# Performance work log

Measured on AMD Instinct MI355X. Metric: run time of the kernel, lower is better.

## Reference

```python
import jax, jax.numpy as jnp
import numpy as np

N_NODES = 100000
N_FEAT = 512
HIDDEN = 256
N_CLASSES = 40
N_EDGES = 1600000
K = 10
ALPHA = 0.1


def setup_inputs() -> dict:
    key = jax.random.key(0)
    ks = jax.random.split(key, 8)
    feat = jax.random.normal(ks[0], (N_NODES, N_FEAT), dtype=jnp.float32)
    src = jax.random.randint(ks[1], (N_EDGES,), 0, N_NODES, dtype=jnp.int32)
    dst = jax.random.randint(ks[2], (N_EDGES,), 0, N_NODES, dtype=jnp.int32)
    # linear layers (PyTorch-style uniform init)
    s1 = 1.0 / np.sqrt(N_FEAT)
    W1 = jax.random.uniform(ks[3], (N_FEAT, HIDDEN), minval=-s1, maxval=s1, dtype=jnp.float32)
    b1 = jax.random.uniform(ks[4], (HIDDEN,), minval=-s1, maxval=s1, dtype=jnp.float32)
    s2 = 1.0 / np.sqrt(HIDDEN)
    W2 = jax.random.uniform(ks[5], (HIDDEN, N_CLASSES), minval=-s2, maxval=s2, dtype=jnp.float32)
    b2 = jax.random.uniform(ks[6], (N_CLASSES,), minval=-s2, maxval=s2, dtype=jnp.float32)
    # PPR init for per-hop weights: temp[k] = alpha*(1-alpha)^k, temp[K] = (1-alpha)^K
    temp = ALPHA * (1.0 - ALPHA) ** np.arange(K + 1)
    temp[-1] = (1.0 - ALPHA) ** K
    temp = jnp.asarray(temp, dtype=jnp.float32)
    return {"feat": feat, "W1": W1, "b1": b1, "W2": W2, "b2": b2,
            "temp": temp, "src": src, "dst": dst}


def reference(feat, W1, b1, W2, b2, temp, src, dst):
    N = feat.shape[0]
    # dgl.add_self_loop
    loop = jnp.arange(N, dtype=src.dtype)
    src_f = jnp.concatenate([src, loop])
    dst_f = jnp.concatenate([dst, loop])
    # MLP: lin1 -> relu -> lin2 (dropout is identity at inference)
    h = jax.nn.relu(feat @ W1 + b1) @ W2 + b2  # [N, C]
    # symmetric normalization: norm_e = d[dst] * d[src], d = deg^{-1/2}
    deg = jax.ops.segment_sum(jnp.ones_like(dst_f, dtype=h.dtype), dst_f, num_segments=N)
    d = jax.lax.rsqrt(deg)  # deg >= 1 due to self loops
    norm = (d[dst_f] * d[src_f])[:, None]  # [E, 1]
    # K-hop propagation with learned per-hop weights
    TH = h * temp[0]
    for k in range(K):
        msg = h[src_f] * norm                     # gather + edge scale
        h = jax.ops.segment_sum(msg, dst_f, num_segments=N)  # scatter-sum
        TH = TH + h * temp[k + 1]
    return jax.nn.log_softmax(TH, axis=1)
```

## Files before the change

kernel.cpp:

```cpp
#include <hip/hip_runtime.h>
#include <math.h>

#define N_NODES 100000
#define N_FEAT  512
#define HIDDEN  256
#define N_CLS   40
#define N_EDGES 1600000
#define K_HOPS  10

#define NPART   8
#define PSZ     12500
#define NPN     (NPART * N_NODES)
#define SCANB   782
#define HROW    40

typedef __attribute__((ext_vector_type(8))) short short8;
typedef __attribute__((ext_vector_type(4))) float f4_t;

__device__ __forceinline__ short f2bf(float f) {
    union { float f; unsigned u; } x; x.f = f;
    unsigned r = x.u + 0x7fffu + ((x.u >> 16) & 1u);
    return (short)(r >> 16);
}

__device__ __forceinline__ float bf2f(short b) {
    union { unsigned u; float f; } x;
    x.u = ((unsigned)(unsigned short)b) << 16;
    return x.f;
}


__global__ __launch_bounds__(256) void init_degp_kernel(int* __restrict__ degp) {
    int idx = blockIdx.x * 256 + threadIdx.x;
    if (idx < NPN) {
        int v = idx >> 3, p = idx & 7;
        degp[idx] = (p == v / PSZ) ? 1 : 0;
    }
}

__global__ __launch_bounds__(256) void count_dst_kernel(const int* __restrict__ src,
                                                        const int* __restrict__ dst,
                                                        int* __restrict__ degp) {
    int e = blockIdx.x * 256 + threadIdx.x;
    if (e < N_EDGES) atomicAdd(&degp[dst[e] * NPART + src[e] / PSZ], 1);
}

__global__ __launch_bounds__(256) void rsqrt_deg_kernel(const int* __restrict__ degp,
                                                        float* __restrict__ d) {
    int v = blockIdx.x * 256 + threadIdx.x;
    if (v < N_NODES) {
        int s = 0;
#pragma unroll
        for (int p = 0; p < NPART; ++p) s += degp[v * NPART + p];
        d[v] = rsqrtf((float)s);
    }
}


__global__ __launch_bounds__(1024) void scan_partial_kernel(const int* __restrict__ degp,
                                                            int* __restrict__ blocksum) {
    __shared__ int s[1024];
    int t = threadIdx.x;
    int idx = blockIdx.x * 1024 + t;
    s[t] = (idx < NPN) ? degp[idx] : 0;
    __syncthreads();
#pragma unroll
    for (int off = 512; off > 0; off >>= 1) {
        if (t < off) s[t] += s[t + off];
        __syncthreads();
    }
    if (t == 0) blocksum[blockIdx.x] = s[0];
}

__global__ __launch_bounds__(1024) void scan_blocks_kernel(const int* __restrict__ blocksum,
                                                           int* __restrict__ blockoff) {
    __shared__ int s[1024];
    int t = threadIdx.x;
    int v = (t < SCANB) ? blocksum[t] : 0;
    s[t] = v;
    __syncthreads();
#pragma unroll
    for (int off = 1; off < 1024; off <<= 1) {
        int add = (t >= off) ? s[t - off] : 0;
        __syncthreads();
        s[t] += add;
        __syncthreads();
    }
    if (t < SCANB) blockoff[t] = s[t] - v;
}

__global__ __launch_bounds__(1024) void scan_write_kernel(const int* __restrict__ degp,
                                                          const int* __restrict__ blockoff,
                                                          int* __restrict__ rowptrp,
                                                          int* __restrict__ cursor) {
    __shared__ int s[1024];
    int t = threadIdx.x;
    int idx = blockIdx.x * 1024 + t;
    int v = (idx < NPN) ? degp[idx] : 0;
    s[t] = v;
    __syncthreads();
#pragma unroll
    for (int off = 1; off < 1024; off <<= 1) {
        int add = (t >= off) ? s[t - off] : 0;
        __syncthreads();
        s[t] += add;
        __syncthreads();
    }
    int pre = s[t] - v + blockoff[blockIdx.x];
    if (idx <= NPN) rowptrp[idx] = pre;
    if (idx < NPN) cursor[idx] = pre;
}

__global__ __launch_bounds__(256) void scatter_edges_kernel(const int* __restrict__ src,
                                                            const int* __restrict__ dst,
                                                            const float* __restrict__ d,
                                                            int* __restrict__ cursor,
                                                            int2* __restrict__ epair) {
    int e = blockIdx.x * 256 + threadIdx.x;
    if (e >= N_EDGES) return;
    int u = src[e], v = dst[e];
    int pos = atomicAdd(&cursor[v * NPART + u / PSZ], 1);
    int2 p;
    p.x = u;
    p.y = __float_as_int(d[u] * d[v]);
    epair[pos] = p;
}

__global__ __launch_bounds__(256) void scatter_self_kernel(const float* __restrict__ d,
                                                           int* __restrict__ cursor,
                                                           int2* __restrict__ epair) {
    int v = blockIdx.x * 256 + threadIdx.x;
    if (v >= N_NODES) return;
    int pos = atomicAdd(&cursor[v * NPART + v / PSZ], 1);
    float dv = d[v];
    int2 p;
    p.x = v;
    p.y = __float_as_int(dv * dv);
    epair[pos] = p;
}

__global__ __launch_bounds__(256) void cvt_w1_kernel(const float* __restrict__ W1,
                                                     short* __restrict__ W1T) {
    int lin = blockIdx.x * 256 + threadIdx.x;
    int k = lin >> 8, n = lin & 255;
    W1T[n * 512 + k] = f2bf(W1[lin]);
}

__global__ __launch_bounds__(256) void cvt_w2_kernel(const float* __restrict__ W2,
                                                     short* __restrict__ W2T) {
    int lin = blockIdx.x * 256 + threadIdx.x;
    int n = lin >> 8, k = lin & 255;
    W2T[lin] = (n < N_CLS) ? f2bf(W2[k * N_CLS + n]) : (short)0;
}

__global__ __launch_bounds__(256, 3) void mlp_kernel(const float* __restrict__ feat,
                                                     const short* __restrict__ W1T,
                                                     const float* __restrict__ b1,
                                                     const short* __restrict__ W2T,
                                                     const float* __restrict__ b2,
                                                     const float* __restrict__ temp,
                                                     short* __restrict__ h,
                                                     float* __restrict__ TH) {
    __shared__ short A[2][64][72];
    __shared__ short sH[64][264];

    const int tid = threadIdx.x;
    const int rbase = blockIdx.x * 64;
    const int lane = tid & 63;
    const int wv = tid >> 6;
    const int quad = lane >> 4;
    const int l15 = lane & 15;

    f4_t acc[4][4];
#pragma unroll
    for (int m = 0; m < 4; ++m)
#pragma unroll
        for (int n = 0; n < 4; ++n) acc[m][n] = (f4_t)0.f;

    const int arow = tid >> 2;
    const int akq = tid & 3;
    const int grow = rbase + arow;
    const bool rv = (grow < N_NODES);
    const float* fp = feat + (size_t)(rv ? grow : 0) * N_FEAT + akq * 16;

    f4_t fA[2][4];
#pragma unroll
    for (int b = 0; b < 2; ++b)
#pragma unroll
        for (int q = 0; q < 4; ++q) fA[b][q] = (f4_t)0.f;
    if (rv) {
        const f4_t* p0 = (const f4_t*)fp;
        const f4_t* p1 = (const f4_t*)(fp + 64);
#pragma unroll
        for (int q = 0; q < 4; ++q) { fA[0][q] = p0[q]; fA[1][q] = p1[q]; }
    }

#pragma unroll
    for (int kt = 0; kt < 8; ++kt) {
        const int b = kt & 1;
        {
            short8 lo, hi;
            lo[0]=f2bf(fA[b][0][0]); lo[1]=f2bf(fA[b][0][1]);
            lo[2]=f2bf(fA[b][0][2]); lo[3]=f2bf(fA[b][0][3]);
            lo[4]=f2bf(fA[b][1][0]); lo[5]=f2bf(fA[b][1][1]);
            lo[6]=f2bf(fA[b][1][2]); lo[7]=f2bf(fA[b][1][3]);
            hi[0]=f2bf(fA[b][2][0]); hi[1]=f2bf(fA[b][2][1]);
            hi[2]=f2bf(fA[b][2][2]); hi[3]=f2bf(fA[b][2][3]);
            hi[4]=f2bf(fA[b][3][0]); hi[5]=f2bf(fA[b][3][1]);
            hi[6]=f2bf(fA[b][3][2]); hi[7]=f2bf(fA[b][3][3]);
            short8* dstp = (short8*)&A[b][arow][akq * 16];
            dstp[0] = lo; dstp[1] = hi;
        }
        __syncthreads();
        if (kt < 6 && rv) {
            const f4_t* p = (const f4_t*)(fp + (kt + 2) * 64);
#pragma unroll
            for (int q = 0; q < 4; ++q) fA[b][q] = p[q];
        }
        const short* wb = W1T + kt * 64;
#pragma unroll
        for (int kk = 0; kk < 64; kk += 32) {
            short8 af[4], bf[4];
#pragma unroll
            for (int n = 0; n < 4; ++n)
                bf[n] = *(const short8*)(wb + (wv * 64 + n * 16 + l15) * 512 +
                                         kk + quad * 8);
#pragma unroll
            for (int m = 0; m < 4; ++m)
                af[m] = *(const short8*)&A[b][m * 16 + l15][kk + quad * 8];
#pragma unroll
            for (int m = 0; m < 4; ++m)
#pragma unroll
                for (int n = 0; n < 4; ++n)
                    acc[m][n] = __builtin_amdgcn_mfma_f32_16x16x32_bf16(af[m], bf[n],
                                                                        acc[m][n], 0, 0, 0);
        }
    }

#pragma unroll
    for (int n = 0; n < 4; ++n) {
        int col = wv * 64 + n * 16 + l15;
        float bb = b1[col];
#pragma unroll
        for (int m = 0; m < 4; ++m)
#pragma unroll
            for (int r = 0; r < 4; ++r) {
                float v = acc[m][n][r] + bb;
                sH[m * 16 + quad * 4 + r][col] = f2bf(v > 0.f ? v : 0.f);
            }
    }
    __syncthreads();

    f4_t accB[3];
#pragma unroll
    for (int n = 0; n < 3; ++n) accB[n] = (f4_t)0.f;
#pragma unroll
    for (int kk = 0; kk < 256; kk += 32) {
        short8 a = *(const short8*)&sH[wv * 16 + l15][kk + quad * 8];
#pragma unroll
        for (int n = 0; n < 3; ++n) {
            short8 b = *(const short8*)(W2T + (n * 16 + l15) * 256 + kk + quad * 8);
            accB[n] = __builtin_amdgcn_mfma_f32_16x16x32_bf16(a, b, accB[n], 0, 0, 0);
        }
    }
    float t0 = temp[0];
#pragma unroll
    for (int n = 0; n < 3; ++n) {
        int col = n * 16 + l15;
        if (col < N_CLS) {
            float bb = b2[col];
#pragma unroll
            for (int r = 0; r < 4; ++r) {
                int grow2 = rbase + wv * 16 + quad * 4 + r;
                if (grow2 < N_NODES) {
                    float v = accB[n][r] + bb;
                    h[(size_t)grow2 * HROW + col] = f2bf(v);
                    TH[grow2 * N_CLS + col] = t0 * v;
                }
            }
        }
    }
}

__global__ __launch_bounds__(256) void prop_kernel(const short* __restrict__ h,
                                                   short* __restrict__ hn,
                                                   const int* __restrict__ rowptrp,
                                                   const int2* __restrict__ epair,
                                                   float* __restrict__ TH,
                                                   const float* __restrict__ temp,
                                                   int kidx) {
    int gid = blockIdx.x * 256 + threadIdx.x;
    int v = gid / 5;
    if (v >= N_NODES) return;
    int c = gid - v * 5;
    int s = __builtin_nontemporal_load(rowptrp + v * NPART);
    int e = __builtin_nontemporal_load(rowptrp + v * NPART + NPART);
    const short* hc = h + c * 8;
    f4_t a0 = (f4_t)0.f, a1 = (f4_t)0.f;
    int j = s;
    for (; j + 4 <= e; j += 4) {
        long long r0 = __builtin_nontemporal_load((const long long*)(epair + j));
        long long r1 = __builtin_nontemporal_load((const long long*)(epair + j + 1));
        long long r2 = __builtin_nontemporal_load((const long long*)(epair + j + 2));
        long long r3 = __builtin_nontemporal_load((const long long*)(epair + j + 3));
        short8 h0 = *(const short8*)(hc + (size_t)(int)r0 * HROW);
        short8 h1 = *(const short8*)(hc + (size_t)(int)r1 * HROW);
        short8 h2 = *(const short8*)(hc + (size_t)(int)r2 * HROW);
        short8 h3 = *(const short8*)(hc + (size_t)(int)r3 * HROW);
        float w0 = __int_as_float((int)(r0 >> 32)), w1 = __int_as_float((int)(r1 >> 32));
        float w2 = __int_as_float((int)(r2 >> 32)), w3 = __int_as_float((int)(r3 >> 32));
#pragma unroll
        for (int i = 0; i < 4; ++i) {
            a0[i] += w0 * bf2f(h0[i]) + w1 * bf2f(h1[i]) + w2 * bf2f(h2[i]) +
                     w3 * bf2f(h3[i]);
            a1[i] += w0 * bf2f(h0[4 + i]) + w1 * bf2f(h1[4 + i]) + w2 * bf2f(h2[4 + i]) +
                     w3 * bf2f(h3[4 + i]);
        }
    }
    for (; j < e; ++j) {
        long long r = __builtin_nontemporal_load((const long long*)(epair + j));
        short8 hb8 = *(const short8*)(hc + (size_t)(int)r * HROW);
        float w = __int_as_float((int)(r >> 32));
#pragma unroll
        for (int i = 0; i < 4; ++i) {
            a0[i] += w * bf2f(hb8[i]);
            a1[i] += w * bf2f(hb8[4 + i]);
        }
    }
    float tk = temp[kidx];
    short8 ob;
#pragma unroll
    for (int i = 0; i < 4; ++i) { ob[i] = f2bf(a0[i]); ob[4 + i] = f2bf(a1[i]); }
    __builtin_nontemporal_store(ob, (short8*)(hn + (size_t)v * HROW + c * 8));
    float* pt = TH + (size_t)v * N_CLS + c * 8;
    f4_t t0 = __builtin_nontemporal_load((const f4_t*)pt);
    f4_t t1 = __builtin_nontemporal_load(((const f4_t*)pt) + 1);
    t0 += tk * a0;
    t1 += tk * a1;
    __builtin_nontemporal_store(t0, (f4_t*)pt);
    __builtin_nontemporal_store(t1, ((f4_t*)pt) + 1);
}

__global__ __launch_bounds__(256) void lsm_kernel(float* __restrict__ out) {
    int wid = (blockIdx.x * 256 + threadIdx.x) >> 6;
    int lane = threadIdx.x & 63;
    if (wid >= N_NODES) return;
    float x = (lane < N_CLS) ? out[wid * N_CLS + lane] : -INFINITY;
    float m = x;
#pragma unroll
    for (int o = 32; o > 0; o >>= 1) m = fmaxf(m, __shfl_xor(m, o, 64));
    float e = (lane < N_CLS) ? expf(x - m) : 0.f;
    float s = e;
#pragma unroll
    for (int o = 32; o > 0; o >>= 1) s += __shfl_xor(s, o, 64);
    float r = x - m - logf(s);
    if (lane < N_CLS) out[wid * N_CLS + lane] = r;
}


extern "C" void kernel_launch(void* const* d_in, const int* in_sizes, int n_in,
                              void* d_out, int out_size, void* d_ws, size_t ws_size,
                              hipStream_t stream) {
    const float* feat = (const float*)d_in[0];
    const float* W1   = (const float*)d_in[1];
    const float* b1   = (const float*)d_in[2];
    const float* W2   = (const float*)d_in[3];
    const float* b2   = (const float*)d_in[4];
    const float* temp = (const float*)d_in[5];
    const int*   src  = (const int*)d_in[6];
    const int*   dst  = (const int*)d_in[7];
    float* out = (float*)d_out;

    char* ws = (char*)d_ws;
    int*   degp    = (int*)(ws + 0);
    short* W1T     = (short*)(ws + 0);
    short* W2T     = (short*)(ws + 262144);
    float* dnorm   = (float*)(ws + 3200000);
    int*   rowptrp = (int*)(ws + 3600000);
    int*   cursor  = (int*)(ws + 6800016);
    int2*  epair   = (int2*)(ws + 10000016);
    short* h0      = (short*)(ws + 23600016);
    short* h1      = (short*)(ws + 31600016);
    int*   blocksum = (int*)(ws + 39600016);
    int*   blockoff = (int*)(ws + 39603152);

    init_degp_kernel<<<(NPN + 255) / 256, 256, 0, stream>>>(degp);
    count_dst_kernel<<<(N_EDGES + 255) / 256, 256, 0, stream>>>(src, dst, degp);
    rsqrt_deg_kernel<<<(N_NODES + 255) / 256, 256, 0, stream>>>(degp, dnorm);
    scan_partial_kernel<<<SCANB, 1024, 0, stream>>>(degp, blocksum);
    scan_blocks_kernel<<<1, 1024, 0, stream>>>(blocksum, blockoff);
    scan_write_kernel<<<SCANB, 1024, 0, stream>>>(degp, blockoff, rowptrp, cursor);
    cvt_w1_kernel<<<512, 256, 0, stream>>>(W1, W1T);
    cvt_w2_kernel<<<64, 256, 0, stream>>>(W2, W2T);
    scatter_edges_kernel<<<(N_EDGES + 255) / 256, 256, 0, stream>>>(src, dst, dnorm, cursor,
                                                                    epair);
    scatter_self_kernel<<<(N_NODES + 255) / 256, 256, 0, stream>>>(dnorm, cursor, epair);

    mlp_kernel<<<(N_NODES + 63) / 64, 256, 0, stream>>>(feat, W1T, b1, W2T, b2, temp, h0, out);

    short* hc = h0;
    short* hn = h1;
    for (int k = 0; k < K_HOPS; ++k) {
        prop_kernel<<<(N_NODES * 5 + 255) / 256, 256, 0, stream>>>(hc, hn, rowptrp, epair,
                                                                   out, temp, k + 1);
        short* t = hc; hc = hn; hn = t;
    }

    lsm_kernel<<<(N_NODES / 4), 256, 0, stream>>>(out);
}
```

Measured before the change: 1.010 ms.

## Stage MLP input via direct-to-LDS loads and batch prop edges through shared memory

The MLP kernel now copies fp32 feature tiles straight into a swizzled LDS buffer with global_load_lds and converts them to bf16 at fragment-read time with packed convert instructions. It also stages outputs through LDS for coalesced stores and raises the occupancy hint. The prop kernel now assigns 51 nodes per block and cooperatively loads each block's contiguous edge list into shared memory, with edge source indices pre-scaled to byte offsets. Nontemporal hints are dropped. These changes aim to cut global load latency and uncoalesced traffic, at the cost of more barriers and LDS pressure, and one idle thread per prop block.

```diff
diff --git a/kernel.cpp b/kernel.cpp
--- a/kernel.cpp
+++ b/kernel.cpp
@@ -1,5 +1,6 @@
 #include <hip/hip_runtime.h>
 #include <math.h>
+#include <stdint.h>
 
 #define N_NODES 100000
 #define N_FEAT  512
@@ -14,6 +15,10 @@
 #define SCANB   782
 #define HROW    40
 
+#define PB      51
+#define PGRID   ((N_NODES + PB - 1) / PB)
+#define ECAP    2048
+
 typedef __attribute__((ext_vector_type(8))) short short8;
 typedef __attribute__((ext_vector_type(4))) float f4_t;
 
@@ -27,6 +32,18 @@
     union { unsigned u; float f; } x;
     x.u = ((unsigned)(unsigned short)b) << 16;
     return x.f;
+}
+
+__device__ __forceinline__ unsigned cvtpk(float lo, float hi) {
+    unsigned r;
+    asm("v_cvt_pk_bf16_f32 %0, %1, %2" : "=v"(r) : "v"(lo), "v"(hi));
+    return r;
+}
+
+__device__ __forceinline__ void gload_lds16(const float* g, void* l) {
+    __builtin_amdgcn_global_load_lds(
+        (const __attribute__((address_space(1))) void*)g,
+        (__attribute__((address_space(3))) void*)l, 16, 0, 0);
 }
 
 
@@ -121,7 +138,7 @@
     int u = src[e], v = dst[e];
     int pos = atomicAdd(&cursor[v * NPART + u / PSZ], 1);
     int2 p;
-    p.x = u;
+    p.x = u * 80;
     p.y = __float_as_int(d[u] * d[v]);
     epair[pos] = p;
 }
@@ -134,7 +151,7 @@
     int pos = atomicAdd(&cursor[v * NPART + v / PSZ], 1);
     float dv = d[v];
     int2 p;
-    p.x = v;
+    p.x = v * 80;
     p.y = __float_as_int(dv * dv);
     epair[pos] = p;
 }
@@ -153,7 +170,7 @@
     W2T[lin] = (n < N_CLS) ? f2bf(W2[k * N_CLS + n]) : (short)0;
 }
 
-__global__ __launch_bounds__(256, 3) void mlp_kernel(const float* __restrict__ feat,
+__global__ __launch_bounds__(256, 4) void mlp_kernel(const float* __restrict__ feat,
                                                      const short* __restrict__ W1T,
                                                      const float* __restrict__ b1,
                                                      const short* __restrict__ W2T,
@@ -161,8 +178,11 @@
                                                      const float* __restrict__ temp,
                                                      short* __restrict__ h,
                                                      float* __restrict__ TH) {
-    __shared__ short A[2][64][72];
-    __shared__ short sH[64][264];
+    __shared__ union {
+        float Af[2][64][64];
+        short sH[64][264];
+        struct { short Ho[64][40]; float To[64][40]; } o;
+    } S;
 
     const int tid = threadIdx.x;
     const int rbase = blockIdx.x * 64;
@@ -177,65 +197,73 @@
 #pragma unroll
         for (int n = 0; n < 4; ++n) acc[m][n] = (f4_t)0.f;
 
-    const int arow = tid >> 2;
-    const int akq = tid & 3;
-    const int grow = rbase + arow;
-    const bool rv = (grow < N_NODES);
-    const float* fp = feat + (size_t)(rv ? grow : 0) * N_FEAT + akq * 16;
-
-    f4_t fA[2][4];
-#pragma unroll
-    for (int b = 0; b < 2; ++b)
-#pragma unroll
-        for (int q = 0; q < 4; ++q) fA[b][q] = (f4_t)0.f;
-    if (rv) {
-        const f4_t* p0 = (const f4_t*)fp;
-        const f4_t* p1 = (const f4_t*)(fp + 64);
-#pragma unroll
-        for (int q = 0; q < 4; ++q) { fA[0][q] = p0[q]; fA[1][q] = p1[q]; }
-    }
-
-#pragma unroll
+    const int sr = tid >> 4;
+    const int su = tid & 15;
+
+#define STAGE(BUF, KT)                                                          \
+    {                                                                           \
+        _Pragma("unroll")                                                       \
+        for (int i = 0; i < 4; ++i) {                                           \
+            int r = i * 16 + sr;                                                \
+            int grow = rbase + r;                                               \
+            if (grow >= N_NODES) grow = N_NODES - 1;                            \
+            int usrc = su ^ (r & 15);                                           \
+            const float* gp = feat + (size_t)grow * N_FEAT + (KT) * 64 + usrc * 4; \
+            gload_lds16(gp, (char*)&S.Af[BUF][0][0] + (i * 256 + tid) * 16);    \
+        }                                                                       \
+    }
+
+    STAGE(0, 0);
+
+#pragma unroll 1
     for (int kt = 0; kt < 8; ++kt) {
         const int b = kt & 1;
-        {
-            short8 lo, hi;
-            lo[0]=f2bf(fA[b][0][0]); lo[1]=f2bf(fA[b][0][1]);
-            lo[2]=f2bf(fA[b][0][2]); lo[3]=f2bf(fA[b][0][3]);
-            lo[4]=f2bf(fA[b][1][0]); lo[5]=f2bf(fA[b][1][1]);
-            lo[6]=f2bf(fA[b][1][2]); lo[7]=f2bf(fA[b][1][3]);
-            hi[0]=f2bf(fA[b][2][0]); hi[1]=f2bf(fA[b][2][1]);
-            hi[2]=f2bf(fA[b][2][2]); hi[3]=f2bf(fA[b][2][3]);
-            hi[4]=f2bf(fA[b][3][0]); hi[5]=f2bf(fA[b][3][1]);
-            hi[6]=f2bf(fA[b][3][2]); hi[7]=f2bf(fA[b][3][3]);
-            short8* dstp = (short8*)&A[b][arow][akq * 16];
-            dstp[0] = lo; dstp[1] = hi;
-        }
-        __syncthreads();
-        if (kt < 6 && rv) {
-            const f4_t* p = (const f4_t*)(fp + (kt + 2) * 64);
-#pragma unroll
-            for (int q = 0; q < 4; ++q) fA[b][q] = p[q];
-        }
+        short8 bfr[2][4];
         const short* wb = W1T + kt * 64;
 #pragma unroll
-        for (int kk = 0; kk < 64; kk += 32) {
-            short8 af[4], bf[4];
+        for (int kk2 = 0; kk2 < 2; ++kk2)
 #pragma unroll
             for (int n = 0; n < 4; ++n)
-                bf[n] = *(const short8*)(wb + (wv * 64 + n * 16 + l15) * 512 +
-                                         kk + quad * 8);
+                bfr[kk2][n] = *(const short8*)(wb + (wv * 64 + n * 16 + l15) * 512 +
+                                               kk2 * 32 + quad * 8);
+        __builtin_amdgcn_sched_barrier(0);
+        if (kt < 7) {
+            STAGE(b ^ 1, kt + 1);
+            asm volatile("s_waitcnt vmcnt(4)" ::: "memory");
+        } else {
+            asm volatile("s_waitcnt vmcnt(0)" ::: "memory");
+        }
+        __builtin_amdgcn_sched_barrier(0);
+        __builtin_amdgcn_s_barrier();
+        __builtin_amdgcn_sched_barrier(0);
+
+#pragma unroll
+        for (int kk2 = 0; kk2 < 2; ++kk2) {
+            short8 af[4];
+#pragma unroll
+            for (int m = 0; m < 4; ++m) {
+                int row = m * 16 + l15;
+                int u0 = (kk2 << 3) + (quad << 1);
+                f4_t lo = *(const f4_t*)&S.Af[b][row][((u0) ^ l15) << 2];
+                f4_t hi = *(const f4_t*)&S.Af[b][row][((u0 + 1) ^ l15) << 2];
+                union { unsigned u[4]; short8 s; } x;
+                x.u[0] = cvtpk(lo[0], lo[1]);
+                x.u[1] = cvtpk(lo[2], lo[3]);
+                x.u[2] = cvtpk(hi[0], hi[1]);
+                x.u[3] = cvtpk(hi[2], hi[3]);
+                af[m] = x.s;
+            }
 #pragma unroll
             for (int m = 0; m < 4; ++m)
-                af[m] = *(const short8*)&A[b][m * 16 + l15][kk + quad * 8];
-#pragma unroll
-            for (int m = 0; m < 4; ++m)
 #pragma unroll
                 for (int n = 0; n < 4; ++n)
-                    acc[m][n] = __builtin_amdgcn_mfma_f32_16x16x32_bf16(af[m], bf[n],
-                                                                        acc[m][n], 0, 0, 0);
-        }
-    }
+                    acc[m][n] = __builtin_amdgcn_mfma_f32_16x16x32_bf16(
+                        af[m], bfr[kk2][n], acc[m][n], 0, 0, 0);
+        }
+        __builtin_amdgcn_sched_barrier(0);
+        __builtin_amdgcn_s_barrier();
+    }
+#undef STAGE
 
 #pragma unroll
     for (int n = 0; n < 4; ++n) {
@@ -246,7 +274,7 @@
 #pragma unroll
             for (int r = 0; r < 4; ++r) {
                 float v = acc[m][n][r] + bb;
-                sH[m * 16 + quad * 4 + r][col] = f2bf(v > 0.f ? v : 0.f);
+                S.sH[m * 16 + quad * 4 + r][col] = f2bf(v > 0.f ? v : 0.f);
             }
     }
     __syncthreads();
@@ -256,13 +284,15 @@
     for (int n = 0; n < 3; ++n) accB[n] = (f4_t)0.f;
 #pragma unroll
     for (int kk = 0; kk < 256; kk += 32) {
-        short8 a = *(const short8*)&sH[wv * 16 + l15][kk + quad * 8];
+        short8 a = *(const short8*)&S.sH[wv * 16 + l15][kk + quad * 8];
 #pragma unroll
         for (int n = 0; n < 3; ++n) {
             short8 b = *(const short8*)(W2T + (n * 16 + l15) * 256 + kk + quad * 8);
             accB[n] = __builtin_amdgcn_mfma_f32_16x16x32_bf16(a, b, accB[n], 0, 0, 0);
         }
     }
+    __syncthreads();
+
     float t0 = temp[0];
 #pragma unroll
     for (int n = 0; n < 3; ++n) {
@@ -271,74 +301,106 @@
             float bb = b2[col];
 #pragma unroll
             for (int r = 0; r < 4; ++r) {
-                int grow2 = rbase + wv * 16 + quad * 4 + r;
-                if (grow2 < N_NODES) {
-                    float v = accB[n][r] + bb;
-                    h[(size_t)grow2 * HROW + col] = f2bf(v);
-                    TH[grow2 * N_CLS + col] = t0 * v;
-                }
+                int row = wv * 16 + quad * 4 + r;
+                float v = accB[n][r] + bb;
+                S.o.Ho[row][col] = f2bf(v);
+                S.o.To[row][col] = t0 * v;
             }
         }
     }
-}
-
-__global__ __launch_bounds__(256) void prop_kernel(const short* __restrict__ h,
-                                                   short* __restrict__ hn,
-                                                   const int* __restrict__ rowptrp,
-                                                   const int2* __restrict__ epair,
-                                                   float* __restrict__ TH,
-                                                   const float* __restrict__ temp,
-                                                   int kidx) {
-    int gid = blockIdx.x * 256 + threadIdx.x;
-    int v = gid / 5;
-    if (v >= N_NODES) return;
-    int c = gid - v * 5;
-    int s = __builtin_nontemporal_load(rowptrp + v * NPART);
-    int e = __builtin_nontemporal_load(rowptrp + v * NPART + NPART);
-    const short* hc = h + c * 8;
+    __syncthreads();
+
+    int rows = N_NODES - rbase; if (rows > 64) rows = 64;
+    int nh = rows * 5;
+    for (int i = tid; i < nh; i += 256)
+        *(short8*)(h + (size_t)rbase * HROW + i * 8) =
+            *(const short8*)((const short*)&S.o.Ho[0][0] + i * 8);
+    int nt = rows * 10;
+    for (int i = tid; i < nt; i += 256)
+        *(f4_t*)(TH + (size_t)rbase * N_CLS + i * 4) =
+            *(const f4_t*)((const float*)&S.o.To[0][0] + i * 4);
+}
+
+__global__ __launch_bounds__(256, 8) void prop_kernel(const short* __restrict__ h,
+                                                      short* __restrict__ hn,
+                                                      const int* __restrict__ rowptrp,
+                                                      const int2* __restrict__ epair,
+                                                      float* __restrict__ TH,
+                                                      const float* __restrict__ temp,
+                                                      int kidx) {
+    __shared__ long long sE[ECAP];
+    __shared__ int sRP[64];
+
+    const int t = threadIdx.x;
+    const int v0 = blockIdx.x * PB;
+    int nmax = N_NODES - v0; if (nmax > PB) nmax = PB;
+    if (t <= nmax) sRP[t] = rowptrp[(v0 + t) * NPART];
+    __syncthreads();
+    const int S0 = sRP[0];
+    const int count = sRP[nmax] - S0;
+
+    const int n = t / 5;
+    const int c = t - n * 5;
+    const bool act = (n < nmax) && (t < 255);
+    const int js = act ? (sRP[n] - S0) : 0;
+    const int je = act ? (sRP[n + 1] - S0) : 0;
+    const char* hB = (const char*)h + c * 16;
+
     f4_t a0 = (f4_t)0.f, a1 = (f4_t)0.f;
-    int j = s;
-    for (; j + 4 <= e; j += 4) {
-        long long r0 = __builtin_nontemporal_load((const long long*)(epair + j));
-        long long r1 = __builtin_nontemporal_load((const long long*)(epair + j + 1));
-        long long r2 = __builtin_nontemporal_load((const long long*)(epair + j + 2));
-        long long r3 = __builtin_nontemporal_load((const long long*)(epair + j + 3));
-        short8 h0 = *(const short8*)(hc + (size_t)(int)r0 * HROW);
-        short8 h1 = *(const short8*)(hc + (size_t)(int)r1 * HROW);
-        short8 h2 = *(const short8*)(hc + (size_t)(int)r2 * HROW);
-        short8 h3 = *(const short8*)(hc + (size_t)(int)r3 * HROW);
-        float w0 = __int_as_float((int)(r0 >> 32)), w1 = __int_as_float((int)(r1 >> 32));
-        float w2 = __int_as_float((int)(r2 >> 32)), w3 = __int_as_float((int)(r3 >> 32));
-#pragma unroll
-        for (int i = 0; i < 4; ++i) {
-            a0[i] += w0 * bf2f(h0[i]) + w1 * bf2f(h1[i]) + w2 * bf2f(h2[i]) +
-                     w3 * bf2f(h3[i]);
-            a1[i] += w0 * bf2f(h0[4 + i]) + w1 * bf2f(h1[4 + i]) + w2 * bf2f(h2[4 + i]) +
-                     w3 * bf2f(h3[4 + i]);
-        }
-    }
-    for (; j < e; ++j) {
-        long long r = __builtin_nontemporal_load((const long long*)(epair + j));
-        short8 hb8 = *(const short8*)(hc + (size_t)(int)r * HROW);
-        float w = __int_as_float((int)(r >> 32));
-#pragma unroll
-        for (int i = 0; i < 4; ++i) {
-            a0[i] += w * bf2f(hb8[i]);
-            a1[i] += w * bf2f(hb8[4 + i]);
-        }
-    }
+    int j = js;
+    for (int base = 0; base < count; base += ECAP) {
+        int lim = count - base; if (lim > ECAP) lim = ECAP;
+        __syncthreads();
+        for (int i = t; i < lim; i += 256)
+            sE[i] = *(const long long*)(epair + (size_t)(S0 + base + i));
+        __syncthreads();
+        int jend = je - base; if (jend > lim) jend = lim;
+        int jj = j - base;
+        for (; jj + 4 <= jend; jj += 4) {
+            long long r0 = sE[jj], r1 = sE[jj + 1], r2 = sE[jj + 2], r3 = sE[jj + 3];
+            short8 h0 = *(const short8*)(hB + (unsigned)(int)r0);
+            short8 h1 = *(const short8*)(hB + (unsigned)(int)r1);
+            short8 h2 = *(const short8*)(hB + (unsigned)(int)r2);
+            short8 h3 = *(const short8*)(hB + (unsigned)(int)r3);
+            float w0 = __int_as_float((int)(r0 >> 32));
+            float w1 = __int_as_float((int)(r1 >> 32));
+            float w2 = __int_as_float((int)(r2 >> 32));
+            float w3 = __int_as_float((int)(r3 >> 32));
+#pragma unroll
+            for (int i = 0; i < 4; ++i) {
+                a0[i] += w0 * bf2f(h0[i]) + w1 * bf2f(h1[i]) + w2 * bf2f(h2[i]) +
+                         w3 * bf2f(h3[i]);
+                a1[i] += w0 * bf2f(h0[4 + i]) + w1 * bf2f(h1[4 + i]) +
+                         w2 * bf2f(h2[4 + i]) + w3 * bf2f(h3[4 + i]);
+            }
+        }
+        for (; jj < jend; ++jj) {
+            long long r = sE[jj];
+            short8 hb8 = *(const short8*)(hB + (unsigned)(int)r);
+            float w = __int_as_float((int)(r >> 32));
+#pragma unroll
+            for (int i = 0; i < 4; ++i) {
+                a0[i] += w * bf2f(hb8[i]);
+                a1[i] += w * bf2f(hb8[4 + i]);
+            }
+        }
+        if (jend > 0 && j < base + jend) j = base + jend;
+    }
+
+    if (!act) return;
+    int v = v0 + n;
     float tk = temp[kidx];
     short8 ob;
 #pragma unroll
     for (int i = 0; i < 4; ++i) { ob[i] = f2bf(a0[i]); ob[4 + i] = f2bf(a1[i]); }
-    __builtin_nontemporal_store(ob, (short8*)(hn + (size_t)v * HROW + c * 8));
+    *(short8*)(hn + (size_t)v * HROW + c * 8) = ob;
     float* pt = TH + (size_t)v * N_CLS + c * 8;
-    f4_t t0 = __builtin_nontemporal_load((const f4_t*)pt);
-    f4_t t1 = __builtin_nontemporal_load(((const f4_t*)pt) + 1);
-    t0 += tk * a0;
-    t1 += tk * a1;
-    __builtin_nontemporal_store(t0, (f4_t*)pt);
-    __builtin_nontemporal_store(t1, ((f4_t*)pt) + 1);
+    f4_t t0v = *(const f4_t*)pt;
+    f4_t t1v = *(((const f4_t*)pt) + 1);
+    t0v += tk * a0;
+    t1v += tk * a1;
+    *(f4_t*)pt = t0v;
+    *(((f4_t*)pt) + 1) = t1v;
 }
 
 __global__ __launch_bounds__(256) void lsm_kernel(float* __restrict__ out) {
@@ -401,8 +463,7 @@
     short* hc = h0;
     short* hn = h1;
     for (int k = 0; k < K_HOPS; ++k) {
-        prop_kernel<<<(N_NODES * 5 + 255) / 256, 256, 0, stream>>>(hc, hn, rowptrp, epair,
-                                                                   out, temp, k + 1);
+        prop_kernel<<<PGRID, 256, 0, stream>>>(hc, hn, rowptrp, epair, out, temp, k + 1);
         short* t = hc; hc = hn; hn = t;
     }
 
```

Measured after the change: 852.5 us. 15.6% less time.
